# Optimization experiments

Measured on AMD Instinct MI355X. Metric: run time of the kernel, lower is better.

Reference implementation:

```python
import jax, jax.numpy as jnp
import numpy as np
import math

B, N, NBS, E, H = 64, 512, 8, 2048, 128
L, K = 3, 4
AF, BF = 82, 6
NA, NBTAB = 100, 10
ALPHA, LAMDA = 0.1, 0.5


def _gelu(x):
    return jax.nn.gelu(x, approximate=False)


def _mask_softmax(a, mask):
    # a: [..., n], mask broadcastable to a; matches torch mask_softmax (eps=1e-6)
    a_exp = jnp.exp(a - jnp.max(a, -1, keepdims=True)) * mask
    return a_exp / (jnp.sum(a_exp, -1, keepdims=True) + 1e-6)


def _gru(x, h, wih, whh, bih, bhh):
    # torch.nn.GRUCell semantics; wih/whh: [3H, H] in (r, z, n) order
    gi = x @ wih.T + bih
    gh = h @ whh.T + bhh
    ir, iz, inn = jnp.split(gi, 3, -1)
    hr, hz, hn = jnp.split(gh, 3, -1)
    r = jax.nn.sigmoid(ir + hr)
    z = jax.nn.sigmoid(iz + hz)
    n = jnp.tanh(inn + r * hn)
    return (1 - z) * n + z * h


def setup_inputs() -> dict:
    key = jax.random.key(0)
    ks = iter(jax.random.split(key, 64))
    def nrm(shape, s=0.05):
        return jax.random.normal(next(ks), shape, dtype=jnp.float32) * s
    def zb(shape):
        return jnp.zeros(shape, jnp.float32)
    inp = dict(
        batch_size=B,
        vertex_mask=jnp.ones((B, N), jnp.float32),
        vertex=jax.random.randint(next(ks), (B, N), 0, NA),
        edge=jax.random.randint(next(ks), (B, E), 0, NBTAB),
        atom_adj=jax.random.randint(next(ks), (B, N, NBS), 0, B * N),
        bond_adj=jax.random.randint(next(ks), (B, N, NBS), 0, B * E),
        nbs_mask=jnp.ones((B, N, NBS), jnp.float32),
        init_atom_features=nrm((NA, AF), 1.0),
        init_bond_features=nrm((NBTAB, BF), 1.0),
        emb_w=nrm((AF, H)), emb_b=zb((H,)),
        u1_w=nrm((L, H + BF, H)), u1_b=zb((L, H)),
        u2_w=nrm((L, 2 * H, H)), u2_b=zb((L, H)),
        fu_w=nrm((L, H, H)), fu_b=zb((L, H)),
        wvm_w=nrm((L, K, H, H)), wvm_b=zb((L, K, H)),
        wmain_w=nrm((L, K, H, H)), wmain_b=zb((L, K, H)),
        wbmm_w=nrm((L, K, H)), wbmm_b=zb((L, K)),
        khead_w=nrm((L, K * H, H)), khead_b=zb((L, H)),
        wmaster_w=nrm((L, H, H)), wmaster_b=zb((L, H)),
        wm2m_w=nrm((L, H, H)), wm2m_b=zb((L, H)),
        wzm1_w=nrm((L, H, H)), wzm1_b=zb((L, H)),
        wzm2_w=nrm((L, H, H)), wzm2_b=zb((L, H)),
        wzs1_w=nrm((L, H, H)), wzs1_b=zb((L, H)),
        wzs2_w=nrm((L, H, H)), wzs2_b=zb((L, H)),
        gru_main_wih=nrm((3 * H, H)), gru_main_whh=nrm((3 * H, H)),
        gru_main_bih=zb((3 * H,)), gru_main_bhh=zb((3 * H,)),
        gru_master_wih=nrm((3 * H, H)), gru_master_whh=nrm((3 * H, H)),
        gru_master_bih=zb((3 * H,)), gru_master_bhh=zb((3 * H,)),
    )
    return inp


def _compute(p, vertex, edge, atom_adj, bond_adj):
    vm = p['vertex_mask']               # [B, N]
    nm = p['nbs_mask']                  # [B, N, NBS]
    b, n_vertex = vm.shape
    nbs = atom_adj.shape[-1]
    # embed initial atom/bond features via table gather
    v_init = p['init_atom_features'][vertex.reshape(-1)].reshape(b, n_vertex, -1)
    e_init = p['init_bond_features'][edge.reshape(-1)].reshape(b, edge.shape[1], -1)
    v_init = v_init * vm[:, :, None]
    vf = _gelu(v_init @ p['emb_w'] + p['emb_b'])                       # [B, N, H]
    h0 = vf
    hdim = vf.shape[-1]
    master = jnp.sum(vf * vm[:, :, None], axis=1, keepdims=True)        # [B, 1, H]
    aa = atom_adj.reshape(-1)
    ba = bond_adj.reshape(-1)
    n_layers = p['u1_w'].shape[0]
    for i in range(n_layers):
        # --- multi-head main -> master attention (all heads vectorized) ---
        mv = jnp.tanh(jnp.einsum('bnh,khd->bknd', vf, p['wvm_w'][i]) + p['wvm_b'][i][None, :, None, :])
        score = jnp.einsum('bknd,kd->bkn', mv * master[:, None, :, :], p['wbmm_w'][i]) + p['wbmm_b'][i][None, :, None]
        att = _mask_softmax(score, vm[:, None, :])                      # [B, K, N]
        proj = jnp.einsum('bnh,khd->bknd', vf, p['wmain_w'][i]) + p['wmain_b'][i][None, :, None, :]
        kmm = jnp.einsum('bkn,bknd->bkd', att, proj)                    # [B, K, H]
        main_to_master = jnp.tanh(kmm.reshape(b, 1, -1) @ p['khead_w'][i] + p['khead_b'][i])  # [B, 1, H]
        # --- GraphConvolution (dropout p = 0.0) ---
        vn = vf.reshape(-1, hdim)[aa].reshape(b, n_vertex, nbs, hdim)
        en = e_init.reshape(-1, e_init.shape[-1])[ba].reshape(b, n_vertex, nbs, -1)
        lab = _gelu(jnp.concatenate([vn, en], -1) @ p['u1_w'][i] + p['u1_b'][i])
        nl = jnp.sum(lab * nm[..., None], axis=-2)                      # [B, N, H]
        hi = jnp.concatenate([nl, vf], -1) @ p['u2_w'][i] + p['u2_b'][i]
        theta = math.log(LAMDA / (i + 1) + 1)
        support = (1 - ALPHA) * hi + ALPHA * h0
        self_vertex = theta * (support @ p['fu_w'][i] + p['fu_b'][i]) + (1 - theta) * support
        # --- master updates + gated mixing + GRU cells ---
        m2m = _gelu(master @ p['wm2m_w'][i] + p['wm2m_b'][i])           # [B, 1, H]
        mself = _gelu(master @ p['wmaster_w'][i] + p['wmaster_b'][i])   # [B, 1, H]
        z_main = jax.nn.sigmoid(self_vertex @ p['wzm1_w'][i] + p['wzm1_b'][i] + m2m @ p['wzm2_w'][i] + p['wzm2_b'][i])
        hidden_main = (1 - z_main) * self_vertex + z_main * m2m          # broadcast [B,N,H]
        vf = _gru(hidden_main.reshape(-1, hdim), vf.reshape(-1, hdim),
                  p['gru_main_wih'], p['gru_main_whh'], p['gru_main_bih'], p['gru_main_bhh']).reshape(b, n_vertex, hdim)
        z_master = jax.nn.sigmoid(mself @ p['wzs1_w'][i] + p['wzs1_b'][i] + main_to_master @ p['wzs2_w'][i] + p['wzs2_b'][i])
        hidden_super = (1 - z_master) * mself + z_master * main_to_master
        master = _gru(hidden_super.reshape(b, hdim), master.reshape(b, hdim),
                      p['gru_master_wih'], p['gru_master_whh'], p['gru_master_bih'], p['gru_master_bhh']).reshape(b, 1, hdim)
    return vf, master


def reference(batch_size, vertex_mask, vertex, edge, atom_adj, bond_adj, nbs_mask,
              init_atom_features, init_bond_features, emb_w, emb_b,
              u1_w, u1_b, u2_w, u2_b, fu_w, fu_b,
              wvm_w, wvm_b, wmain_w, wmain_b, wbmm_w, wbmm_b, khead_w, khead_b,
              wmaster_w, wmaster_b, wm2m_w, wm2m_b,
              wzm1_w, wzm1_b, wzm2_w, wzm2_b, wzs1_w, wzs1_b, wzs2_w, wzs2_b,
              gru_main_wih, gru_main_whh, gru_main_bih, gru_main_bhh,
              gru_master_wih, gru_master_whh, gru_master_bih, gru_master_bhh):
    p = dict(vertex_mask=vertex_mask, nbs_mask=nbs_mask,
             init_atom_features=init_atom_features, init_bond_features=init_bond_features,
             emb_w=emb_w, emb_b=emb_b, u1_w=u1_w, u1_b=u1_b, u2_w=u2_w, u2_b=u2_b,
             fu_w=fu_w, fu_b=fu_b, wvm_w=wvm_w, wvm_b=wvm_b, wmain_w=wmain_w, wmain_b=wmain_b,
             wbmm_w=wbmm_w, wbmm_b=wbmm_b, khead_w=khead_w, khead_b=khead_b,
             wmaster_w=wmaster_w, wmaster_b=wmaster_b, wm2m_w=wm2m_w, wm2m_b=wm2m_b,
             wzm1_w=wzm1_w, wzm1_b=wzm1_b, wzm2_w=wzm2_w, wzm2_b=wzm2_b,
             wzs1_w=wzs1_w, wzs1_b=wzs1_b, wzs2_w=wzs2_w, wzs2_b=wzs2_b,
             gru_main_wih=gru_main_wih, gru_main_whh=gru_main_whh,
             gru_main_bih=gru_main_bih, gru_main_bhh=gru_main_bhh,
             gru_master_wih=gru_master_wih, gru_master_whh=gru_master_whh,
             gru_master_bih=gru_master_bih, gru_master_bhh=gru_master_bhh)
    return _compute(p, vertex, edge, atom_adj, bond_adj)
```

## Files before the change

kernel.cpp:

```cpp
#include <hip/hip_runtime.h>
#include <hip/hip_bf16.h>
#include <cmath>

#define BB 64
#define NN 512
#define NBS 8
#define EE 2048
#define HH 128
#define LL 3
#define KK 4
#define AF 82
#define BF 6
#define SLAB 4194304

typedef __attribute__((ext_vector_type(8))) short bf16x8;
typedef __attribute__((ext_vector_type(4))) float f32x4;

__device__ __forceinline__ float gelu1(float x){ return 0.5f*x*(1.f+erff(x*0.7071067811865475f)); }
__device__ __forceinline__ float sig1(float x){ return 1.f/(1.f+expf(-x)); }
__device__ __forceinline__ short f2bs(float x){ __hip_bfloat16 b=__float2bfloat16(x); return *reinterpret_cast<short*>(&b); }
__device__ __forceinline__ float bs2f(short s){ unsigned u = ((unsigned)(unsigned short)s) << 16; union{unsigned u; float f;} c; c.u=u; return c.f; }
__device__ __forceinline__ void split2(float v, short& hi, short& lo){ hi = f2bs(v); lo = f2bs(v - bs2f(hi)); }

#define MFMA3(ACC, AH, AL, BH, BL) \
// ... 41 lines not shown
                bf16x8 bl = *(const bf16x8*)(bp + 49152);
                MFMA3(acc[nt],   a0h[kc], a0l[kc], bh, bl);
                MFMA3(acc[8+nt], a1h[kc], a1l[kc], bh, bl);
            }
        }
        #pragma unroll
        for (int mt = 0; mt < 2; ++mt)
            #pragma unroll
            for (int nt = 0; nt < 8; ++nt) {
                int col = nt*16 + ml;
                #pragma unroll
                for (int r = 0; r < 4; ++r) {
                    int gm = m0 + mt*16 + quad*4 + r;
                    pvfb[(size_t)gm*128 + col] = f2bs(acc[mt*8+nt][r]);
                }
            }
    } else {
        const int v = bid - 256;
        const int k = v >> 8;
        const int tile = v & 255;
        const int b = tile >> 2;
        const int r0 = tile*128 + wv*32 + ml;
        const int r1 = r0 + 16;

        bf16x8 a0h[4], a0l[4], a1h[4], a1l[4];
        #pragma unroll
        for (int kc = 0; kc < 4; ++kc) {
            const int kq = kc*32 + quad*8;
            a0h[kc] = *(const bf16x8*)(vfh + (size_t)r0*128 + kq);
            a0l[kc] = *(const bf16x8*)(vfl + (size_t)r0*128 + kq);
            a1h[kc] = *(const bf16x8*)(vfh + (size_t)r1*128 + kq);
            a1l[kc] = *(const bf16x8*)(vfl + (size_t)r1*128 + kq);
        }
        f32x4 acc[16];
        #pragma unroll
        for (int i = 0; i < 16; ++i) acc[i] = (f32x4){0.f,0.f,0.f,0.f};
        const short* wcol = wtwvm + (size_t)k*16384 + (size_t)ml*128;
        #pragma unroll
        for (int kc = 0; kc < 4; ++kc) {
            const int kq = kc*32 + quad*8;
            #pragma unroll
            for (int nt = 0; nt < 8; ++nt) {
                const short* bp = wcol + (size_t)nt*16*128 + kq;
                bf16x8 bh = *(const bf16x8*)bp;
                bf16x8 bl = *(const bf16x8*)(bp + 196608);
                MFMA3(acc[nt],   a0h[kc], a0l[kc], bh, bl);
                MFMA3(acc[8+nt], a1h[kc], a1l[kc], bh, bl);
            }
        }
        float wv8[8], bj8[8];
        #pragma unroll
        for (int nt = 0; nt < 8; ++nt) {
            int col = nt*16 + ml;
            wv8[nt] = master[(size_t)b*128 + col] * wbw[(size_t)k*128 + col];
            bj8[nt] = wvmb[(size_t)k*128 + col];
        }
        float kb = wbb[k];
        #pragma unroll
        for (int mt = 0; mt < 2; ++mt) {
            #pragma unroll
            for (int r = 0; r < 4; ++r) {
                float s = 0.f;
                #pragma unroll
                for (int nt = 0; nt < 8; ++nt)
                    s += tanhf(acc[mt*8+nt][r] + bj8[nt]) * wv8[nt];
                s += __shfl_xor(s, 1); s += __shfl_xor(s, 2);
                s += __shfl_xor(s, 4); s += __shfl_xor(s, 8);
                if (ml == 0) {
                    int nloc = (tile & 3)*128 + wv*32 + mt*16 + quad*4 + r;
                    score[((size_t)(b*KK + k))*NN + nloc] = s + kb;
                }
            }
        }
    }
}

__global__ __launch_bounds__(256) void layer_k2(
    const short* __restrict__ pvfb, const float* __restrict__ pet,
    const int* __restrict__ aadj, const int* __restrict__ badj,
    const int* __restrict__ edge, const float* __restrict__ nbm,
    short* __restrict__ nlh, short* __restrict__ nll,
    const float* __restrict__ score, const float* __restrict__ vm,
    const float* __restrict__ vfc,
    float* __restrict__ satt, float* __restrict__ ctx)
{
    __shared__ float smem[768];
    const int bid = blockIdx.x;
    const int t = threadIdx.x;

    if (bid < 8192) {
        const int w = t >> 6, l = t & 63;
        const int i = bid*4 + w;
        const int sg = l >> 4, j = l & 15;
        float acc[8];
        #pragma unroll
        for (int c = 0; c < 8; ++c) acc[c] = 0.f;
        #pragma unroll
        for (int it = 0; it < 2; ++it) {
            int s = it*4 + sg;
            int flat = i*8 + s;
            int g = aadj[flat];
            int eid = edge[badj[flat]];
            float nv = nbm[flat];
            bf16x8 pv8 = *(const bf16x8*)(pvfb + (size_t)g*128 + j*8);
            const float* pp = pet + (size_t)eid*128 + j*8;
            float4 p0 = *(const float4*)pp, p1 = *(const float4*)(pp+4);
            float pe[8] = {p0.x,p0.y,p0.z,p0.w,p1.x,p1.y,p1.z,p1.w};
            #pragma unroll
            for (int c = 0; c < 8; ++c)
                acc[c] += gelu1(bs2f(pv8[c]) + pe[c]) * nv;
        }
        #pragma unroll
        for (int c = 0; c < 8; ++c) {
            acc[c] += __shfl_xor(acc[c], 16);
            acc[c] += __shfl_xor(acc[c], 32);
        }
        if (sg == 0) {
            short hs[8], ls[8];
            #pragma unroll
            for (int c = 0; c < 8; ++c) split2(acc[c], hs[c], ls[c]);
            size_t o = (size_t)i*128 + j*8;
            *(short4*)(nlh + o)     = make_short4(hs[0],hs[1],hs[2],hs[3]);
            *(short4*)(nlh + o + 4) = make_short4(hs[4],hs[5],hs[6],hs[7]);
            *(short4*)(nll + o)     = make_short4(ls[0],ls[1],ls[2],ls[3]);
            *(short4*)(nll + o + 4) = make_short4(ls[4],ls[5],ls[6],ls[7]);
        }
    } else {
        float* red = smem;
        float* att = smem + 256;
        const int bk = bid - 8192, b = bk >> 2;
        float v0 = score[(size_t)bk*NN + t], v1 = score[(size_t)bk*NN + 256 + t];
        red[t] = fmaxf(v0, v1); __syncthreads();
        for (int s = 128; s; s >>= 1) { if (t < s) red[t] = fmaxf(red[t], red[t+s]); __syncthreads(); }
        float mx = red[0]; __syncthreads();
        float e0 = expf(v0 - mx) * vm[b*NN + t];
        float e1 = expf(v1 - mx) * vm[b*NN + t + 256];
        red[t] = e0 + e1; __syncthreads();
        for (int s = 128; s; s >>= 1) { if (t < s) red[t] += red[t+s]; __syncthreads(); }
        float sum = red[0];
        float inv = 1.f / (sum + 1e-6f);
        att[t] = e0*inv; att[t+256] = e1*inv;
        if (t == 0) satt[bk] = sum*inv;
        __syncthreads();
        const int d = t & 127, h = t >> 7;
        float acc = 0.f;
        const float* V = vfc + (size_t)b*NN*HH;
        #pragma unroll 8
        for (int n = h*256; n < h*256 + 256; ++n) acc += att[n]*V[(size_t)n*HH + d];
        red[t] = acc; __syncthreads();
        if (t < 128) ctx[(size_t)bk*HH + t] = red[t] + red[t+128];
    }
}

__global__ __launch_bounds__(256, 2) void layer_k3(
    const short* __restrict__ nlh, const short* __restrict__ nll,
    const float* __restrict__ vfc, const short* __restrict__ vfch, const short* __restrict__ vfcl,
    float* __restrict__ vfn, short* __restrict__ vfnh, short* __restrict__ vfnl,
    const short* __restrict__ h0b,
    const short* __restrict__ wu2, const float* __restrict__ u2b,
    const short* __restrict__ wfu, const float* __restrict__ fub,
    const short* __restrict__ wbc, const float* __restrict__ zmb2v,
    const short* __restrict__ wih, const short* __restrict__ whh,
    const float* __restrict__ bih, const float* __restrict__ bhh,
    const float* __restrict__ t2, const float* __restrict__ m2m,
    float theta,
    const float* __restrict__ ctx, const float* __restrict__ satt,
    float* __restrict__ master,
    const float* __restrict__ wmain_w, const float* __restrict__ wmain_b,
    const float* __restrict__ khead_w, const float* __restrict__ khead_b,
    const float* __restrict__ wmaster_w, const float* __restrict__ wmaster_b,
    const float* __restrict__ wzs1_w,  const float* __restrict__ wzs1_b,
    const float* __restrict__ wzs2_w,  const float* __restrict__ wzs2_b,
    const float* __restrict__ WTih, const float* __restrict__ WThh,
    const float* __restrict__ bihm, const float* __restrict__ bhhm,
    const float* __restrict__ wm2m_n_w, const float* __restrict__ wm2m_n_b,
    const float* __restrict__ wzm2_n_w, const float* __restrict__ wzm2_n_b,
    float* __restrict__ m2m_out, float* __restrict__ t2_out)
{
    __shared__ __align__(16) char smem_raw[34816];
    const int bid = blockIdx.x;
    const int t = threadIdx.x;

    if (bid >= 64) {
        short* sh = (short*)smem_raw;
        short* sl = sh + 64*136;
        const int vb = bid - 64;
        const int lane = t & 63, wv = t >> 6;
        const int quad = lane >> 4, ml = lane & 15;
        const int base = vb * 64;
        const int bb = base >> 9;
        const int c0 = wv*32 + ml;
        const int c1 = c0 + 16;
        const int kq0 = quad*8;

        f32x4 acc[4][2];
        #pragma unroll
        for (int rt = 0; rt < 4; ++rt) {
            acc[rt][0] = (f32x4){0.f,0.f,0.f,0.f};
            acc[rt][1] = (f32x4){0.f,0.f,0.f,0.f};
        }

        #pragma unroll
        for (int kc = 0; kc < 4; ++kc) {
            const int kq = kc*32 + kq0;
            const short* bp0 = wu2 + (size_t)c0*256 + kq;
            const short* bp1 = wu2 + (size_t)c1*256 + kq;
            bf16x8 b0h = *(const bf16x8*)bp0, b0l = *(const bf16x8*)(bp0+98304);
            bf16x8 b1h = *(const bf16x8*)bp1, b1l = *(const bf16x8*)(bp1+98304);
            #pragma unroll
            for (int rt = 0; rt < 4; ++rt) {
                const size_t ar = (size_t)(base + rt*16 + ml);
                bf16x8 ah = *(const bf16x8*)(nlh + ar*128 + kq);
                bf16x8 al = *(const bf16x8*)(nll + ar*128 + kq);
                MFMA3(acc[rt][0], ah, al, b0h, b0l);
                MFMA3(acc[rt][1], ah, al, b1h, b1l);
            }
        }
        #pragma unroll
        for (int kc = 0; kc < 4; ++kc) {
            const int kq = kc*32 + kq0;
            const short* bp0 = wu2 + (size_t)c0*256 + 128 + kq;
            const short* bp1 = wu2 + (size_t)c1*256 + 128 + kq;
            bf16x8 b0h = *(const bf16x8*)bp0, b0l = *(const bf16x8*)(bp0+98304);
            bf16x8 b1h = *(const bf16x8*)bp1, b1l = *(const bf16x8*)(bp1+98304);
            #pragma unroll
            for (int rt = 0; rt < 4; ++rt) {
                const size_t ar = (size_t)(base + rt*16 + ml);
                bf16x8 ah = *(const bf16x8*)(vfch + ar*128 + kq);
                bf16x8 al = *(const bf16x8*)(vfcl + ar*128 + kq);
                MFMA3(acc[rt][0], ah, al, b0h, b0l);
                MFMA3(acc[rt][1], ah, al, b1h, b1l);
            }
        }
        f32x4 sup[4][2];
        {
            const float bj0 = u2b[c0], bj1 = u2b[c1];
            #pragma unroll
            for (int rt = 0; rt < 4; ++rt) {
                #pragma unroll
                for (int r = 0; r < 4; ++r) {
                    const size_t grow = (size_t)(base + rt*16 + quad*4 + r);
                    sup[rt][0][r] = 0.9f*(acc[rt][0][r]+bj0) + 0.1f*bs2f(h0b[grow*128 + c0]);
                    sup[rt][1][r] = 0.9f*(acc[rt][1][r]+bj1) + 0.1f*bs2f(h0b[grow*128 + c1]);
                    const int lrow = rt*16 + quad*4 + r;
                    short h_, l_;
                    split2(sup[rt][0][r], h_, l_); sh[lrow*136 + c0] = h_; sl[lrow*136 + c0] = l_;
                    split2(sup[rt][1][r], h_, l_); sh[lrow*136 + c1] = h_; sl[lrow*136 + c1] = l_;
                }
            }
        }
        __syncthreads();

        f32x4 accz[4][2];
        #pragma unroll
        for (int rt = 0; rt < 4; ++rt) {
            acc[rt][0] = (f32x4){0.f,0.f,0.f,0.f};
            acc[rt][1] = (f32x4){0.f,0.f,0.f,0.f};
            accz[rt][0] = (f32x4){0.f,0.f,0.f,0.f};
            accz[rt][1] = (f32x4){0.f,0.f,0.f,0.f};
        }
        #pragma unroll
        for (int kc = 0; kc < 4; ++kc) {
            const int kq = kc*32 + kq0;
            const short* bp0 = wfu + (size_t)c0*128 + kq;
            const short* bp1 = wfu + (size_t)c1*128 + kq;
            const short* zp0 = wbc + (size_t)c0*128 + kq;
            const short* zp1 = wbc + (size_t)c1*128 + kq;
            bf16x8 b0h = *(const bf16x8*)bp0, b0l = *(const bf16x8*)(bp0+49152);
            bf16x8 b1h = *(const bf16x8*)bp1, b1l = *(const bf16x8*)(bp1+49152);
            bf16x8 z0h = *(const bf16x8*)zp0, z0l = *(const bf16x8*)(zp0+49152);
            bf16x8 z1h = *(const bf16x8*)zp1, z1l = *(const bf16x8*)(zp1+49152);
            #pragma unroll
            for (int rt = 0; rt < 4; ++rt) {
                bf16x8 xh = *(const bf16x8*)&sh[(rt*16+ml)*136 + kq];
                bf16x8 xl = *(const bf16x8*)&sl[(rt*16+ml)*136 + kq];
                MFMA3(acc[rt][0], xh, xl, b0h, b0l);
                MFMA3(acc[rt][1], xh, xl, b1h, b1l);
                MFMA3(accz[rt][0], xh, xl, z0h, z0l);
                MFMA3(accz[rt][1], xh, xl, z1h, z1l);
            }
        }
        f32x4 hid[4][2];
        {
            const float bj0 = fub[c0], bj1 = fub[c1];
            const float zb0 = zmb2v[c0] + t2[(size_t)bb*128 + c0];
            const float zb1 = zmb2v[c1] + t2[(size_t)bb*128 + c1];
            const float m20 = m2m[(size_t)bb*128 + c0], m21 = m2m[(size_t)bb*128 + c1];
            #pragma unroll
            for (int rt = 0; rt < 4; ++rt) {
                #pragma unroll
                for (int r = 0; r < 4; ++r) {
                    float sv0 = theta*(acc[rt][0][r]+bj0) + (1.f-theta)*sup[rt][0][r];
                    float sv1 = theta*(acc[rt][1][r]+bj1) + (1.f-theta)*sup[rt][1][r];
                    float z0 = sig1(accz[rt][0][r] + zb0);
                    float z1 = sig1(accz[rt][1][r] + zb1);
                    hid[rt][0][r] = (1.f-z0)*sv0 + z0*m20;
                    hid[rt][1][r] = (1.f-z1)*sv1 + z1*m21;
                }
            }
        }
        __syncthreads();
        #pragma unroll
        for (int rt = 0; rt < 4; ++rt) {
            #pragma unroll
            for (int r = 0; r < 4; ++r) {
                const int lrow = rt*16 + quad*4 + r;
                short h_, l_;
                split2(hid[rt][0][r], h_, l_); sh[lrow*136 + c0] = h_; sl[lrow*136 + c0] = l_;
                split2(hid[rt][1][r], h_, l_); sh[lrow*136 + c1] = h_; sl[lrow*136 + c1] = l_;
            }
        }
        __syncthreads();

        f32x4 gr[4][2], gi[4][2], gh[4][2];
        #pragma unroll
        for (int rt = 0; rt < 4; ++rt) {
            gr[rt][0] = (f32x4){0.f,0.f,0.f,0.f};
            gr[rt][1] = (f32x4){0.f,0.f,0.f,0.f};
        }
        #pragma unroll
        for (int kc = 0; kc < 4; ++kc) {
            const int kq = kc*32 + kq0;
            const short* pw0 = wih + (size_t)c0*128 + kq;
            const short* pw1 = wih + (size_t)c1*128 + kq;
            const short* pu0 = whh + (size_t)c0*128 + kq;
            const short* pu1 = whh + (size_t)c1*128 + kq;
            bf16x8 w0h=*(const bf16x8*)pw0, w0l=*(const bf16x8*)(pw0+49152);
            bf16x8 w1h=*(const bf16x8*)pw1, w1l=*(const bf16x8*)(pw1+49152);
            bf16x8 u0h=*(const bf16x8*)pu0, u0l=*(const bf16x8*)(pu0+49152);
            bf16x8 u1h=*(const bf16x8*)pu1, u1l=*(const bf16x8*)(pu1+49152);
            #pragma unroll
            for (int rt = 0; rt < 4; ++rt) {
                const size_t ar = (size_t)(base + rt*16 + ml);
                bf16x8 xh = *(const bf16x8*)&sh[(rt*16+ml)*136 + kq];
                bf16x8 xl = *(const bf16x8*)&sl[(rt*16+ml)*136 + kq];
                bf16x8 hh = *(const bf16x8*)(vfch + ar*128 + kq);
                bf16x8 hl = *(const bf16x8*)(vfcl + ar*128 + kq);
                MFMA3(gr[rt][0], xh, xl, w0h, w0l);
                MFMA3(gr[rt][0], hh, hl, u0h, u0l);
                MFMA3(gr[rt][1], xh, xl, w1h, w1l);
                MFMA3(gr[rt][1], hh, hl, u1h, u1l);
            }
        }
        {
            const float br0 = bih[c0] + bhh[c0], br1 = bih[c1] + bhh[c1];
            #pragma unroll
            for (int rt = 0; rt < 4; ++rt) {
                #pragma unroll
                for (int r = 0; r < 4; ++r) {
                    gr[rt][0][r] = sig1(gr[rt][0][r] + br0);
                    gr[rt][1][r] = sig1(gr[rt][1][r] + br1);
                }
            }
        }
        #pragma unroll
        for (int rt = 0; rt < 4; ++rt) {
            gi[rt][0] = (f32x4){0.f,0.f,0.f,0.f};
            gi[rt][1] = (f32x4){0.f,0.f,0.f,0.f};
            gh[rt][0] = (f32x4){0.f,0.f,0.f,0.f};
            gh[rt][1] = (f32x4){0.f,0.f,0.f,0.f};
        }
        #pragma unroll
        for (int kc = 0; kc < 4; ++kc) {
            const int kq = kc*32 + kq0;
            const short* pw0 = wih + (size_t)(256 + c0)*128 + kq;
            const short* pw1 = wih + (size_t)(256 + c1)*128 + kq;
            const short* pu0 = whh + (size_t)(256 + c0)*128 + kq;
            const short* pu1 = whh + (size_t)(256 + c1)*128 + kq;
            bf16x8 w0h=*(const bf16x8*)pw0, w0l=*(const bf16x8*)(pw0+49152);
            bf16x8 w1h=*(const bf16x8*)pw1, w1l=*(const bf16x8*)(pw1+49152);
            bf16x8 u0h=*(const bf16x8*)pu0, u0l=*(const bf16x8*)(pu0+49152);
            bf16x8 u1h=*(const bf16x8*)pu1, u1l=*(const bf16x8*)(pu1+49152);
            #pragma unroll
            for (int rt = 0; rt < 4; ++rt) {
                const size_t ar = (size_t)(base + rt*16 + ml);
                bf16x8 xh = *(const bf16x8*)&sh[(rt*16+ml)*136 + kq];
                bf16x8 xl = *(const bf16x8*)&sl[(rt*16+ml)*136 + kq];
                bf16x8 hh = *(const bf16x8*)(vfch + ar*128 + kq);
                bf16x8 hl = *(const bf16x8*)(vfcl + ar*128 + kq);
                MFMA3(gi[rt][0], xh, xl, w0h, w0l);
                MFMA3(gh[rt][0], hh, hl, u0h, u0l);
                MFMA3(gi[rt][1], xh, xl, w1h, w1l);
                MFMA3(gh[rt][1], hh, hl, u1h, u1l);
            }
        }
        {
            const float bn0 = bih[256+c0], bn1 = bih[256+c1];
            const float un0 = bhh[256+c0], un1 = bhh[256+c1];
            #pragma unroll
            for (int rt = 0; rt < 4; ++rt) {
                #pragma unroll
                for (int r = 0; r < 4; ++r) {
                    gi[rt][0][r] = tanhf(gi[rt][0][r] + bn0 + gr[rt][0][r]*(gh[rt][0][r] + un0));
                    gi[rt][1][r] = tanhf(gi[rt][1][r] + bn1 + gr[rt][1][r]*(gh[rt][1][r] + un1));
                }
            }
        }
        #pragma unroll
        for (int rt = 0; rt < 4; ++rt) {
            gh[rt][0] = (f32x4){0.f,0.f,0.f,0.f};
            gh[rt][1] = (f32x4){0.f,0.f,0.f,0.f};
        }
        #pragma unroll
        for (int kc = 0; kc < 4; ++kc) {
            const int kq = kc*32 + kq0;
            const short* pw0 = wih + (size_t)(128 + c0)*128 + kq;
            const short* pw1 = wih + (size_t)(128 + c1)*128 + kq;
            const short* pu0 = whh + (size_t)(128 + c0)*128 + kq;
            const short* pu1 = whh + (size_t)(128 + c1)*128 + kq;
            bf16x8 w0h=*(const bf16x8*)pw0, w0l=*(const bf16x8*)(pw0+49152);
            bf16x8 w1h=*(const bf16x8*)pw1, w1l=*(const bf16x8*)(pw1+49152);
            bf16x8 u0h=*(const bf16x8*)pu0, u0l=*(const bf16x8*)(pu0+49152);
            bf16x8 u1h=*(const bf16x8*)pu1, u1l=*(const bf16x8*)(pu1+49152);
            #pragma unroll
            for (int rt = 0; rt < 4; ++rt) {
                const size_t ar = (size_t)(base + rt*16 + ml);
                bf16x8 xh = *(const bf16x8*)&sh[(rt*16+ml)*136 + kq];
                bf16x8 xl = *(const bf16x8*)&sl[(rt*16+ml)*136 + kq];
                bf16x8 hh = *(const bf16x8*)(vfch + ar*128 + kq);
                bf16x8 hl = *(const bf16x8*)(vfcl + ar*128 + kq);
                MFMA3(gh[rt][0], xh, xl, w0h, w0l);
                MFMA3(gh[rt][0], hh, hl, u0h, u0l);
                MFMA3(gh[rt][1], xh, xl, w1h, w1l);
                MFMA3(gh[rt][1], hh, hl, u1h, u1l);
            }
        }
        {
            const float bz0 = bih[128+c0] + bhh[128+c0];
            const float bz1 = bih[128+c1] + bhh[128+c1];
            #pragma unroll
            for (int rt = 0; rt < 4; ++rt) {
                #pragma unroll
                for (int r = 0; r < 4; ++r) {
                    const size_t grow = (size_t)(base + rt*16 + quad*4 + r);
                    const size_t off0 = grow*128 + c0, off1 = grow*128 + c1;
                    float z0 = sig1(gh[rt][0][r] + bz0);
                    float z1 = sig1(gh[rt][1][r] + bz1);
                    float o0 = (1.f-z0)*gi[rt][0][r] + z0*vfc[off0];
                    float o1 = (1.f-z1)*gi[rt][1][r] + z1*vfc[off1];
                    vfn[off0] = o0; vfn[off1] = o1;
                    short h_, l_;
                    split2(o0, h_, l_); vfnh[off0] = h_; vfnl[off0] = l_;
                    split2(o1, h_, l_); vfnh[off1] = h_; vfnl[off1] = l_;
                }
            }
        }
    } else {
        float* smemf = (float*)smem_raw;
        float* xs = smemf;
        float* ms = smemf + 512;
        float* msN = smemf + 640;
        float* v_mtm = smemf + 768;
        float* v_mself = smemf + 896;
        float* v_m2m = smemf + 1024;
        float* v_t2 = smemf + 1152;
        float* v_ts1 = smemf + 1280;
        float* v_ts2 = smemf + 1408;
        float* v_hsup = smemf + 1536;
        float* gi = smemf + 1664;
        float* gh2 = smemf + 2048;
        float* red = smemf + 2432;
        const int b = bid;

        if (t < 128) ms[t] = master[(size_t)b*128 + t];
        __syncthreads();

        const int c = t & 127, p = t >> 7;

        #pragma unroll
        for (int k = 0; k < 4; ++k) {
            const float* cx = ctx + ((size_t)b*KK + k)*128;
            const float* Wk = wmain_w + (size_t)k*16384;
            float s = 0.f;
            for (int d = p*64; d < p*64+64; ++d) s += cx[d]*Wk[(size_t)d*128 + c];
            red[t] = s; __syncthreads();
            if (t < 128) xs[k*128 + c] = red[c] + red[c+128] + satt[(size_t)b*KK + k]*wmain_b[k*128 + c];
            __syncthreads();
        }

        auto matvec = [&](const float* src, const float* __restrict__ W,
                          const float* __restrict__ bias, int K, float* out, int act) {
            int half = K >> 1;
            int k0 = p*half, k1 = k0 + half;
            float s = 0.f;
            for (int k = k0; k < k1; ++k) s += src[k]*W[(size_t)k*128 + c];
            red[t] = s; __syncthreads();
            if (t < 128) {
                float v = red[c] + red[c+128] + bias[c];
                if (act == 1) v = gelu1(v); else if (act == 2) v = tanhf(v);
                out[c] = v;
            }
            __syncthreads();
        };

        matvec(xs, khead_w, khead_b, 512, v_mtm, 2);
        matvec(ms, wmaster_w, wmaster_b, 128, v_mself, 1);
        matvec(v_mself, wzs1_w, wzs1_b, 128, v_ts1, 0);
        matvec(v_mtm, wzs2_w, wzs2_b, 128, v_ts2, 0);

        if (t < 128) {
            float z = sig1(v_ts1[t] + v_ts2[t]);
            v_hsup[t] = (1.f-z)*v_mself[t] + z*v_mtm[t];
        }
        __syncthreads();

        for (int j = t; j < 384; j += 256) {
            float a = 0.f, h2 = 0.f;
            for (int k = 0; k < 128; ++k) {
                a  += v_hsup[k]*WTih[(size_t)k*384 + j];
                h2 += ms[k]*WThh[(size_t)k*384 + j];
            }
            gi[j] = a + bihm[j];
            gh2[j] = h2 + bhhm[j];
        }
        __syncthreads();
        if (t < 128) {
            float r = sig1(gi[t] + gh2[t]);
            float z = sig1(gi[128+t] + gh2[128+t]);
            float n = tanhf(gi[256+t] + r*gh2[256+t]);
            float nm = (1.f-z)*n + z*ms[t];
            master[(size_t)b*128 + t] = nm;
            msN[t] = nm;
        }
        __syncthreads();

        matvec(msN, wm2m_n_w, wm2m_n_b, 128, v_m2m, 1);
        matvec(v_m2m, wzm2_n_w, wzm2_n_b, 128, v_t2, 0);
        if (t < 128) {
            m2m_out[(size_t)b*128 + t] = v_m2m[t];
            t2_out[(size_t)b*128 + t]  = v_t2[t];
        }
    }
}

__global__ __launch_bounds__(256) void embed_kernel(
    const float* __restrict__ atomf, const int* __restrict__ vertex,
    const float* __restrict__ vmask,
    const short* __restrict__ WT, const float* __restrict__ bias,
    float* __restrict__ vf, short* __restrict__ h0b,
    short* __restrict__ vfh, short* __restrict__ vfl)
{
    const int t = threadIdx.x;
    const int lane = t & 63, wv = t >> 6;
    const int quad = lane >> 4, ml = lane & 15;
    const int m0 = blockIdx.x*128 + wv*32;
    const int r0 = m0 + ml, r1 = m0 + 16 + ml;
    const int ga0 = vertex[r0], ga1 = vertex[r1];
    const float vm0 = vmask[r0], vm1 = vmask[r1];

    f32x4 acc[16];
    #pragma unroll
    for (int i = 0; i < 16; ++i) acc[i] = (f32x4){0.f,0.f,0.f,0.f};
    const short* wcol = WT + (size_t)ml*96;

    #pragma unroll
    for (int kc = 0; kc < 3; ++kc) {
        const int kq = kc*32 + quad*8;
        float av0[8], av1[8];
        const float* p0r = atomf + (size_t)ga0*AF + kq;
        const float* p1r = atomf + (size_t)ga1*AF + kq;
        #pragma unroll
        for (int j2 = 0; j2 < 4; ++j2) {
            int k = kq + 2*j2;
            if (k + 2 <= AF) {
                float2 v0 = *(const float2*)(p0r + 2*j2);
                float2 v1 = *(const float2*)(p1r + 2*j2);
                av0[2*j2]=v0.x*vm0; av0[2*j2+1]=v0.y*vm0;
                av1[2*j2]=v1.x*vm1; av1[2*j2+1]=v1.y*vm1;
            } else { av0[2*j2]=0.f; av0[2*j2+1]=0.f; av1[2*j2]=0.f; av1[2*j2+1]=0.f; }
        }
        bf16x8 a0h, a0l, a1h, a1l;
        #pragma unroll
        for (int j = 0; j < 8; ++j) {
            short h, l;
            split2(av0[j], h, l); a0h[j]=h; a0l[j]=l;
            split2(av1[j], h, l); a1h[j]=h; a1l[j]=l;
        }
        #pragma unroll
        for (int nt = 0; nt < 8; ++nt) {
            const short* bp = wcol + (size_t)nt*16*96 + kq;
            bf16x8 bh = *(const bf16x8*)bp;
            bf16x8 bl = *(const bf16x8*)(bp + 12288);
            MFMA3(acc[nt],   a0h, a0l, bh, bl);
            MFMA3(acc[8+nt], a1h, a1l, bh, bl);
        }
    }

    #pragma unroll
    for (int mt = 0; mt < 2; ++mt) {
        #pragma unroll
        for (int nt = 0; nt < 8; ++nt) {
            int col = nt*16 + ml;
            float bj = bias[col];
            #pragma unroll
            for (int r = 0; r < 4; ++r) {
                int gm = m0 + mt*16 + quad*4 + r;
                float v = gelu1(acc[mt*8+nt][r] + bj);
                size_t off = (size_t)gm*128 + col;
                vf[off] = v;
                short h_, l_; split2(v, h_, l_);
                vfh[off] = h_; vfl[off] = l_;
                h0b[off] = h_;
            }
        }
    }
}

__global__ __launch_bounds__(256) void master_init_a(
    const float* __restrict__ vf, const float* __restrict__ vm,
    float* __restrict__ master)
{
    __shared__ float red[256];
    const int bid = blockIdx.x;
    const int b = bid >> 3, sl = bid & 7;
    const int t = threadIdx.x;
    const int c = t & 127, half = t >> 7;
    float s = 0.f;
    for (int n = sl*64 + half; n < sl*64 + 64; n += 2)
        s += vf[((size_t)b*NN + n)*HH + c] * vm[b*NN + n];
    red[t] = s; __syncthreads();
    if (t < 128) atomicAdd(&master[(size_t)b*HH + c], red[c] + red[c+128]);
}

__global__ __launch_bounds__(256) void master_init_b(
    const float* __restrict__ master,
    const float* __restrict__ wm2m_w, const float* __restrict__ wm2m_b,
    const float* __restrict__ wzm2_w, const float* __restrict__ wzm2_b,
    float* __restrict__ m2m_out, float* __restrict__ t2_out)
{
    __shared__ float red[256], ms[128], v_m2m[128];
    const int b = blockIdx.x, t = threadIdx.x;
    if (t < 128) ms[t] = master[(size_t)b*HH + t];
    __syncthreads();
    const int c = t & 127, p = t >> 7;
    {
        float s2 = 0.f;
        for (int k = p*64; k < p*64+64; ++k) s2 += ms[k]*wm2m_w[(size_t)k*128 + c];
        red[t] = s2; __syncthreads();
        if (t < 128) { float v = gelu1(red[c] + red[c+128] + wm2m_b[c]); v_m2m[c] = v; m2m_out[(size_t)b*128 + c] = v; }
        __syncthreads();
    }
    {
        float s2 = 0.f;
        for (int k = p*64; k < p*64+64; ++k) s2 += v_m2m[k]*wzm2_w[(size_t)k*128 + c];
        red[t] = s2; __syncthreads();
        if (t < 128) t2_out[(size_t)b*128 + c] = red[c] + red[c+128] + wzm2_b[c];
    }
}

__device__ __forceinline__ void cvt_t2(const float* __restrict__ src, short* __restrict__ dst,
                                       int i, int K, int Kpad, int total, int zrows)
{
    int z = i / (128*Kpad); int rem = i - z*128*Kpad;
    int col = rem / Kpad; int k = rem - col*Kpad;
    float v = (k < K) ? src[(size_t)z*zrows*128 + (size_t)k*128 + col] : 0.f;
    short h, l; split2(v, h, l);
    dst[i] = h; dst[total + i] = l;
}

// ... 43 lines not shown
        const float* fu = fu_w + (size_t)li*16384 + (size_t)k*128;
        const float* wz = wzm1_w + (size_t)li*16384;
        float s = 0.f;
        for (int j = 0; j < 128; ++j) s += fu[j] * wz[(size_t)j*128 + c];
        s = theta*s + (1.f-theta)*wz[(size_t)k*128 + c];
        short h, lo; split2(s, h, lo);
        size_t d = (size_t)li*16384 + (size_t)c*128 + k;
        wt_wbc[d] = h; wt_wbc[49152 + d] = lo;
    }
    else if (i < 704640) {
        int o = i - 704256; int li = o >> 7; int c = o & 127;
        float theta = logf(0.5f/(float)(li+1) + 1.f);
        float s = 0.f;
        for (int j = 0; j < 128; ++j)
            s += fu_bv[li*128 + j] * wzm1_w[(size_t)li*16384 + (size_t)j*128 + c];
        zmb2[o] = wzm1_bv[li*128 + c] + theta*s;
    }
    else if (i < 712832) {
        master0[i - 704640] = 0.f;
    }
}

__global__ void copy_out_kernel(const float* __restrict__ vf, const float* __restrict__ master,
                                float* __restrict__ out)
{
    int i = blockIdx.x*256 + threadIdx.x;
    const int nvf4 = SLAB/4;
    if (i < nvf4) ((float4*)out)[i] = ((const float4*)vf)[i];
    else ((float4*)out)[i] = ((const float4*)master)[i - nvf4];
}

extern "C" void kernel_launch(void* const* d_in, const int* in_sizes, int n_in,
                              void* d_out, int out_size, void* d_ws, size_t ws_size,
                              hipStream_t stream)
{
    (void)in_sizes; (void)n_in; (void)out_size; (void)ws_size;
    const float* vmask = (const float*)d_in[1];
    const int*   vertex= (const int*)d_in[2];
    const int*   edge  = (const int*)d_in[3];
    const int*   aadj  = (const int*)d_in[4];
    const int*   badj  = (const int*)d_in[5];
    const float* nbm   = (const float*)d_in[6];
    const float* atomf = (const float*)d_in[7];
    const float* bondf = (const float*)d_in[8];
    const float* emb_w = (const float*)d_in[9];
    const float* emb_b = (const float*)d_in[10];
    const float* u1_w  = (const float*)d_in[11];
    const float* u1_b  = (const float*)d_in[12];
    const float* u2_w  = (const float*)d_in[13];
    const float* u2_b  = (const float*)d_in[14];
    const float* fu_w  = (const float*)d_in[15];
    const float* fu_b  = (const float*)d_in[16];
    const float* wvm_w = (const float*)d_in[17];
    const float* wvm_b = (const float*)d_in[18];
    const float* wmain_w=(const float*)d_in[19];
    const float* wmain_b=(const float*)d_in[20];
    const float* wbmm_w= (const float*)d_in[21];
    const float* wbmm_b= (const float*)d_in[22];
    const float* khead_w=(const float*)d_in[23];
    const float* khead_b=(const float*)d_in[24];
    const float* wmaster_w=(const float*)d_in[25];
    const float* wmaster_b=(const float*)d_in[26];
    const float* wm2m_w= (const float*)d_in[27];
    const float* wm2m_b= (const float*)d_in[28];
    const float* wzm1_w= (const float*)d_in[29];
    const float* wzm1_b= (const float*)d_in[30];
    const float* wzm2_w= (const float*)d_in[31];
    const float* wzm2_b= (const float*)d_in[32];
    const float* wzs1_w= (const float*)d_in[33];
    const float* wzs1_b= (const float*)d_in[34];
    const float* wzs2_w= (const float*)d_in[35];
    const float* wzs2_b= (const float*)d_in[36];
    const float* g_wih = (const float*)d_in[37];
    const float* g_whh = (const float*)d_in[38];
    const float* g_bih = (const float*)d_in[39];
    const float* g_bhh = (const float*)d_in[40];
    const float* gm_wih= (const float*)d_in[41];
    const float* gm_whh= (const float*)d_in[42];
    const float* gm_bih= (const float*)d_in[43];
    const float* gm_bhh= (const float*)d_in[44];

    float* ws     = (float*)d_ws;
    float* vfA    = ws;
    float* vfB    = vfA + SLAB;
    float* score  = vfB + SLAB;
    float* ctx    = score + BB*KK*NN;
    float* satt   = ctx + BB*KK*HH;
    float* master = satt + BB*KK;
    float* m2mA   = master + BB*HH;
    float* t2A    = m2mA + BB*HH;
    float* m2mB   = t2A + BB*HH;
    float* t2B    = m2mB + BB*HH;
    float* WTih_s = t2B + BB*HH;
    float* WThh_s = WTih_s + 128*384;
    float* pet    = WThh_s + 128*384;
    short* vfhA   = (short*)(pet + 3840);
    short* vflA   = vfhA + SLAB;
    short* vfhB   = vflA + SLAB;
    short* vflB   = vfhB + SLAB;
    short* nlh    = vflB + SLAB;
    short* nll    = nlh + SLAB;
    short* pvfb   = nll + SLAB;
    short* h0b    = pvfb + SLAB;
    short* wt_emb   = h0b + SLAB;
    short* wt_wvm   = wt_emb   + 2*12288;
    short* wt_pv    = wt_wvm   + 2*196608;
    short* wt_u2    = wt_pv    + 2*49152;
    short* wt_fu    = wt_u2    + 2*98304;
    short* wt_wzm1  = wt_fu    + 2*49152;
    short* wt_gih   = wt_wzm1  + 2*49152;
    short* wt_ghh   = wt_gih   + 2*49152;
    short* wt_wbc   = wt_ghh   + 2*49152;
    float* zmb2     = (float*)(wt_wbc + 2*49152);

    wprep_kernel<<<2785, 256, 0, stream>>>(
        emb_w, wvm_w, u1_w, u1_b, u2_w, fu_w, fu_b, wzm1_w, wzm1_b,
        g_wih, g_whh, gm_wih, gm_whh, bondf,
        wt_emb, wt_wvm, wt_pv, wt_u2, wt_fu, wt_wzm1, wt_gih, wt_ghh,
        wt_wbc, zmb2, WTih_s, WThh_s, pet, master);

    embed_kernel<<<256, 256, 0, stream>>>(atomf, vertex, vmask, wt_emb, emb_b,
                                          vfA, h0b, vfhA, vflA);

    master_init_a<<<512, 256, 0, stream>>>(vfA, vmask, master);
    master_init_b<<<BB, 256, 0, stream>>>(master, wm2m_w, wm2m_b, wzm2_w, wzm2_b,
                                          m2mA, t2A);

    for (int i = 0; i < LL; ++i) {
        float theta = logf(0.5f/(float)(i+1) + 1.f);
        const bool even = (i % 2 == 0);
        float* vfc  = even ? vfA  : vfB;
        short* vfch = even ? vfhA : vfhB;
        short* vfcl = even ? vflA : vflB;
        float* vfn  = even ? vfB  : vfA;
        short* vfnh = even ? vfhB : vfhA;
        short* vfnl = even ? vflB : vflA;
        float* m2mR = even ? m2mA : m2mB;
        float* t2R  = even ? t2A  : t2B;
        float* m2mW = even ? m2mB : m2mA;
        float* t2W  = even ? t2B  : t2A;
        int nx = (i+1 < LL) ? i+1 : i;

        layer_k1<<<1280, 256, 0, stream>>>(
            vfch, vfcl,
            wt_pv + (size_t)i*16384, pvfb,
            wt_wvm + (size_t)i*4*16384, wvm_b + (size_t)i*4*128,
            master, wbmm_w + (size_t)i*KK*HH, wbmm_b + (size_t)i*KK, score);

        layer_k2<<<8448, 256, 0, stream>>>(
            pvfb, pet + (size_t)i*1280,
            aadj, badj, edge, nbm, nlh, nll,
            score, vmask, vfc, satt, ctx);

        layer_k3<<<576, 256, 0, stream>>>(
            nlh, nll, vfc, vfch, vfcl, vfn, vfnh, vfnl, h0b,
            wt_u2 + (size_t)i*128*256, u2_b + i*HH,
            wt_fu + (size_t)i*16384, fu_b + i*HH,
            wt_wbc + (size_t)i*16384, zmb2 + i*HH,
            wt_gih, wt_ghh, g_bih, g_bhh,
            t2R, m2mR, theta,
            ctx, satt, master,
            wmain_w + (size_t)i*KK*HH*HH, wmain_b + (size_t)i*KK*HH,
            khead_w + (size_t)i*KK*HH*HH, khead_b + i*HH,
            wmaster_w + (size_t)i*HH*HH, wmaster_b + i*HH,
            wzs1_w + (size_t)i*HH*HH, wzs1_b + i*HH,
            wzs2_w + (size_t)i*HH*HH, wzs2_b + i*HH,
            WTih_s, WThh_s, gm_bih, gm_bhh,
            wm2m_w + (size_t)nx*HH*HH, wm2m_b + nx*HH,
            wzm2_w + (size_t)nx*HH*HH, wzm2_b + nx*HH,
            m2mW, t2W);
    }

    copy_out_kernel<<<(SLAB + BB*HH)/4/256, 256, 0, stream>>>(vfB, master, (float*)d_out);
}
```

Measured before the change: 783.0 us.

## Double layer_k3 block size so each wave computes one 16-column tile

layer_k3 now launches 512 threads per block instead of 256. In the MFMA path each of the eight waves computes one 16-column slice of the 64-row tile instead of two, which halves per-thread accumulator registers and spreads the weight loads over more waves. The master-node matvec path splits its K reduction four ways instead of two. This is meant to raise parallelism and latency hiding per block. In exchange, more waves share the same shared-memory activation loads, and the 34.8 KB shared buffer and red array must hold 512 entries.

```diff
diff --git a/kernel.cpp b/kernel.cpp
--- a/kernel.cpp
+++ b/kernel.cpp
@@ -217,7 +217,7 @@
     }
 }
 
-__global__ __launch_bounds__(256, 2) void layer_k3(
+__global__ __launch_bounds__(512) void layer_k3(
     const short* __restrict__ nlh, const short* __restrict__ nll,
     const float* __restrict__ vfc, const short* __restrict__ vfch, const short* __restrict__ vfcl,
     float* __restrict__ vfn, short* __restrict__ vfnh, short* __restrict__ vfnl,
@@ -254,113 +254,89 @@
         const int quad = lane >> 4, ml = lane & 15;
         const int base = vb * 64;
         const int bb = base >> 9;
-        const int c0 = wv*32 + ml;
-        const int c1 = c0 + 16;
+        const int c0 = wv*16 + ml;
         const int kq0 = quad*8;
 
-        f32x4 acc[4][2];
-        #pragma unroll
-        for (int rt = 0; rt < 4; ++rt) {
-            acc[rt][0] = (f32x4){0.f,0.f,0.f,0.f};
-            acc[rt][1] = (f32x4){0.f,0.f,0.f,0.f};
-        }
+        f32x4 acc[4];
+        #pragma unroll
+        for (int rt = 0; rt < 4; ++rt) acc[rt] = (f32x4){0.f,0.f,0.f,0.f};
 
         #pragma unroll
         for (int kc = 0; kc < 4; ++kc) {
             const int kq = kc*32 + kq0;
             const short* bp0 = wu2 + (size_t)c0*256 + kq;
-            const short* bp1 = wu2 + (size_t)c1*256 + kq;
             bf16x8 b0h = *(const bf16x8*)bp0, b0l = *(const bf16x8*)(bp0+98304);
-            bf16x8 b1h = *(const bf16x8*)bp1, b1l = *(const bf16x8*)(bp1+98304);
             #pragma unroll
             for (int rt = 0; rt < 4; ++rt) {
                 const size_t ar = (size_t)(base + rt*16 + ml);
                 bf16x8 ah = *(const bf16x8*)(nlh + ar*128 + kq);
                 bf16x8 al = *(const bf16x8*)(nll + ar*128 + kq);
-                MFMA3(acc[rt][0], ah, al, b0h, b0l);
-                MFMA3(acc[rt][1], ah, al, b1h, b1l);
+                MFMA3(acc[rt], ah, al, b0h, b0l);
             }
         }
         #pragma unroll
         for (int kc = 0; kc < 4; ++kc) {
             const int kq = kc*32 + kq0;
             const short* bp0 = wu2 + (size_t)c0*256 + 128 + kq;
-            const short* bp1 = wu2 + (size_t)c1*256 + 128 + kq;
             bf16x8 b0h = *(const bf16x8*)bp0, b0l = *(const bf16x8*)(bp0+98304);
-            bf16x8 b1h = *(const bf16x8*)bp1, b1l = *(const bf16x8*)(bp1+98304);
             #pragma unroll
             for (int rt = 0; rt < 4; ++rt) {
                 const size_t ar = (size_t)(base + rt*16 + ml);
                 bf16x8 ah = *(const bf16x8*)(vfch + ar*128 + kq);
                 bf16x8 al = *(const bf16x8*)(vfcl + ar*128 + kq);
-                MFMA3(acc[rt][0], ah, al, b0h, b0l);
-                MFMA3(acc[rt][1], ah, al, b1h, b1l);
-            }
-        }
-        f32x4 sup[4][2];
+                MFMA3(acc[rt], ah, al, b0h, b0l);
+            }
+        }
+        f32x4 sup[4];
         {
-            const float bj0 = u2b[c0], bj1 = u2b[c1];
+            const float bj0 = u2b[c0];
             #pragma unroll
             for (int rt = 0; rt < 4; ++rt) {
                 #pragma unroll
                 for (int r = 0; r < 4; ++r) {
                     const size_t grow = (size_t)(base + rt*16 + quad*4 + r);
-                    sup[rt][0][r] = 0.9f*(acc[rt][0][r]+bj0) + 0.1f*bs2f(h0b[grow*128 + c0]);
-                    sup[rt][1][r] = 0.9f*(acc[rt][1][r]+bj1) + 0.1f*bs2f(h0b[grow*128 + c1]);
+                    sup[rt][r] = 0.9f*(acc[rt][r]+bj0) + 0.1f*bs2f(h0b[grow*128 + c0]);
                     const int lrow = rt*16 + quad*4 + r;
                     short h_, l_;
-                    split2(sup[rt][0][r], h_, l_); sh[lrow*136 + c0] = h_; sl[lrow*136 + c0] = l_;
-                    split2(sup[rt][1][r], h_, l_); sh[lrow*136 + c1] = h_; sl[lrow*136 + c1] = l_;
+                    split2(sup[rt][r], h_, l_); sh[lrow*136 + c0] = h_; sl[lrow*136 + c0] = l_;
                 }
             }
         }
         __syncthreads();
 
-        f32x4 accz[4][2];
+        f32x4 accz[4];
         #pragma unroll
         for (int rt = 0; rt < 4; ++rt) {
-            acc[rt][0] = (f32x4){0.f,0.f,0.f,0.f};
-            acc[rt][1] = (f32x4){0.f,0.f,0.f,0.f};
-            accz[rt][0] = (f32x4){0.f,0.f,0.f,0.f};
-            accz[rt][1] = (f32x4){0.f,0.f,0.f,0.f};
+            acc[rt] = (f32x4){0.f,0.f,0.f,0.f};
+            accz[rt] = (f32x4){0.f,0.f,0.f,0.f};
         }
         #pragma unroll
         for (int kc = 0; kc < 4; ++kc) {
             const int kq = kc*32 + kq0;
             const short* bp0 = wfu + (size_t)c0*128 + kq;
-            const short* bp1 = wfu + (size_t)c1*128 + kq;
             const short* zp0 = wbc + (size_t)c0*128 + kq;
-            const short* zp1 = wbc + (size_t)c1*128 + kq;
             bf16x8 b0h = *(const bf16x8*)bp0, b0l = *(const bf16x8*)(bp0+49152);
-            bf16x8 b1h = *(const bf16x8*)bp1, b1l = *(const bf16x8*)(bp1+49152);
             bf16x8 z0h = *(const bf16x8*)zp0, z0l = *(const bf16x8*)(zp0+49152);
-            bf16x8 z1h = *(const bf16x8*)zp1, z1l = *(const bf16x8*)(zp1+49152);
             #pragma unroll
             for (int rt = 0; rt < 4; ++rt) {
                 bf16x8 xh = *(const bf16x8*)&sh[(rt*16+ml)*136 + kq];
                 bf16x8 xl = *(const bf16x8*)&sl[(rt*16+ml)*136 + kq];
-                MFMA3(acc[rt][0], xh, xl, b0h, b0l);
-                MFMA3(acc[rt][1], xh, xl, b1h, b1l);
-                MFMA3(accz[rt][0], xh, xl, z0h, z0l);
-                MFMA3(accz[rt][1], xh, xl, z1h, z1l);
-            }
-        }
-        f32x4 hid[4][2];
+                MFMA3(acc[rt], xh, xl, b0h, b0l);
+                MFMA3(accz[rt], xh, xl, z0h, z0l);
+            }
+        }
+        f32x4 hid[4];
         {
-            const float bj0 = fub[c0], bj1 = fub[c1];
+            const float bj0 = fub[c0];
             const float zb0 = zmb2v[c0] + t2[(size_t)bb*128 + c0];
-            const float zb1 = zmb2v[c1] + t2[(size_t)bb*128 + c1];
-            const float m20 = m2m[(size_t)bb*128 + c0], m21 = m2m[(size_t)bb*128 + c1];
+            const float m20 = m2m[(size_t)bb*128 + c0];
             #pragma unroll
             for (int rt = 0; rt < 4; ++rt) {
                 #pragma unroll
                 for (int r = 0; r < 4; ++r) {
-                    float sv0 = theta*(acc[rt][0][r]+bj0) + (1.f-theta)*sup[rt][0][r];
-                    float sv1 = theta*(acc[rt][1][r]+bj1) + (1.f-theta)*sup[rt][1][r];
-                    float z0 = sig1(accz[rt][0][r] + zb0);
-                    float z1 = sig1(accz[rt][1][r] + zb1);
-                    hid[rt][0][r] = (1.f-z0)*sv0 + z0*m20;
-                    hid[rt][1][r] = (1.f-z1)*sv1 + z1*m21;
+                    float sv0 = theta*(acc[rt][r]+bj0) + (1.f-theta)*sup[rt][r];
+                    float z0 = sig1(accz[rt][r] + zb0);
+                    hid[rt][r] = (1.f-z0)*sv0 + z0*m20;
                 }
             }
         }
@@ -371,29 +347,21 @@
             for (int r = 0; r < 4; ++r) {
                 const int lrow = rt*16 + quad*4 + r;
                 short h_, l_;
-                split2(hid[rt][0][r], h_, l_); sh[lrow*136 + c0] = h_; sl[lrow*136 + c0] = l_;
-                split2(hid[rt][1][r], h_, l_); sh[lrow*136 + c1] = h_; sl[lrow*136 + c1] = l_;
+                split2(hid[rt][r], h_, l_); sh[lrow*136 + c0] = h_; sl[lrow*136 + c0] = l_;
             }
         }
         __syncthreads();
 
-        f32x4 gr[4][2], gi[4][2], gh[4][2];
-        #pragma unroll
-        for (int rt = 0; rt < 4; ++rt) {
-            gr[rt][0] = (f32x4){0.f,0.f,0.f,0.f};
-            gr[rt][1] = (f32x4){0.f,0.f,0.f,0.f};
-        }
+        f32x4 gr[4], gi[4], gh[4];
+        #pragma unroll
+        for (int rt = 0; rt < 4; ++rt) gr[rt] = (f32x4){0.f,0.f,0.f,0.f};
         #pragma unroll
         for (int kc = 0; kc < 4; ++kc) {
             const int kq = kc*32 + kq0;
             const short* pw0 = wih + (size_t)c0*128 + kq;
-            const short* pw1 = wih + (size_t)c1*128 + kq;
             const short* pu0 = whh + (size_t)c0*128 + kq;
-            const short* pu1 = whh + (size_t)c1*128 + kq;
             bf16x8 w0h=*(const bf16x8*)pw0, w0l=*(const bf16x8*)(pw0+49152);
-            bf16x8 w1h=*(const bf16x8*)pw1, w1l=*(const bf16x8*)(pw1+49152);
             bf16x8 u0h=*(const bf16x8*)pu0, u0l=*(const bf16x8*)(pu0+49152);
-            bf16x8 u1h=*(const bf16x8*)pu1, u1l=*(const bf16x8*)(pu1+49152);
             #pragma unroll
             for (int rt = 0; rt < 4; ++rt) {
                 const size_t ar = (size_t)(base + rt*16 + ml);
@@ -401,41 +369,30 @@
                 bf16x8 xl = *(const bf16x8*)&sl[(rt*16+ml)*136 + kq];
                 bf16x8 hh = *(const bf16x8*)(vfch + ar*128 + kq);
                 bf16x8 hl = *(const bf16x8*)(vfcl + ar*128 + kq);
-                MFMA3(gr[rt][0], xh, xl, w0h, w0l);
-                MFMA3(gr[rt][0], hh, hl, u0h, u0l);
-                MFMA3(gr[rt][1], xh, xl, w1h, w1l);
-                MFMA3(gr[rt][1], hh, hl, u1h, u1l);
+                MFMA3(gr[rt], xh, xl, w0h, w0l);
+                MFMA3(gr[rt], hh, hl, u0h, u0l);
             }
         }
         {
-            const float br0 = bih[c0] + bhh[c0], br1 = bih[c1] + bhh[c1];
-            #pragma unroll
-            for (int rt = 0; rt < 4; ++rt) {
+            const float br0 = bih[c0] + bhh[c0];
+            #pragma unroll
+            for (int rt = 0; rt < 4; ++rt)
                 #pragma unroll
-                for (int r = 0; r < 4; ++r) {
-                    gr[rt][0][r] = sig1(gr[rt][0][r] + br0);
-                    gr[rt][1][r] = sig1(gr[rt][1][r] + br1);
-                }
-            }
+                for (int r = 0; r < 4; ++r)
+                    gr[rt][r] = sig1(gr[rt][r] + br0);
         }
         #pragma unroll
         for (int rt = 0; rt < 4; ++rt) {
-            gi[rt][0] = (f32x4){0.f,0.f,0.f,0.f};
-            gi[rt][1] = (f32x4){0.f,0.f,0.f,0.f};
-            gh[rt][0] = (f32x4){0.f,0.f,0.f,0.f};
-            gh[rt][1] = (f32x4){0.f,0.f,0.f,0.f};
+            gi[rt] = (f32x4){0.f,0.f,0.f,0.f};
+            gh[rt] = (f32x4){0.f,0.f,0.f,0.f};
         }
         #pragma unroll
         for (int kc = 0; kc < 4; ++kc) {
             const int kq = kc*32 + kq0;
             const short* pw0 = wih + (size_t)(256 + c0)*128 + kq;
-            const short* pw1 = wih + (size_t)(256 + c1)*128 + kq;
             const short* pu0 = whh + (size_t)(256 + c0)*128 + kq;
-            const short* pu1 = whh + (size_t)(256 + c1)*128 + kq;
             bf16x8 w0h=*(const bf16x8*)pw0, w0l=*(const bf16x8*)(pw0+49152);
-            bf16x8 w1h=*(const bf16x8*)pw1, w1l=*(const bf16x8*)(pw1+49152);
             bf16x8 u0h=*(const bf16x8*)pu0, u0l=*(const bf16x8*)(pu0+49152);
-            bf16x8 u1h=*(const bf16x8*)pu1, u1l=*(const bf16x8*)(pu1+49152);
             #pragma unroll
             for (int rt = 0; rt < 4; ++rt) {
                 const size_t ar = (size_t)(base + rt*16 + ml);
@@ -443,40 +400,28 @@
                 bf16x8 xl = *(const bf16x8*)&sl[(rt*16+ml)*136 + kq];
                 bf16x8 hh = *(const bf16x8*)(vfch + ar*128 + kq);
                 bf16x8 hl = *(const bf16x8*)(vfcl + ar*128 + kq);
-                MFMA3(gi[rt][0], xh, xl, w0h, w0l);
-                MFMA3(gh[rt][0], hh, hl, u0h, u0l);
-                MFMA3(gi[rt][1], xh, xl, w1h, w1l);
-                MFMA3(gh[rt][1], hh, hl, u1h, u1l);
+                MFMA3(gi[rt], xh, xl, w0h, w0l);
+                MFMA3(gh[rt], hh, hl, u0h, u0l);
             }
         }
         {
-            const float bn0 = bih[256+c0], bn1 = bih[256+c1];
-            const float un0 = bhh[256+c0], un1 = bhh[256+c1];
-            #pragma unroll
-            for (int rt = 0; rt < 4; ++rt) {
+            const float bn0 = bih[256+c0];
+            const float un0 = bhh[256+c0];
+            #pragma unroll
+            for (int rt = 0; rt < 4; ++rt)
                 #pragma unroll
-                for (int r = 0; r < 4; ++r) {
-                    gi[rt][0][r] = tanhf(gi[rt][0][r] + bn0 + gr[rt][0][r]*(gh[rt][0][r] + un0));
-                    gi[rt][1][r] = tanhf(gi[rt][1][r] + bn1 + gr[rt][1][r]*(gh[rt][1][r] + un1));
-                }
-            }
-        }
-        #pragma unroll
-        for (int rt = 0; rt < 4; ++rt) {
-            gh[rt][0] = (f32x4){0.f,0.f,0.f,0.f};
-            gh[rt][1] = (f32x4){0.f,0.f,0.f,0.f};
-        }
+                for (int r = 0; r < 4; ++r)
+                    gi[rt][r] = tanhf(gi[rt][r] + bn0 + gr[rt][r]*(gh[rt][r] + un0));
+        }
+        #pragma unroll
+        for (int rt = 0; rt < 4; ++rt) gh[rt] = (f32x4){0.f,0.f,0.f,0.f};
         #pragma unroll
         for (int kc = 0; kc < 4; ++kc) {
             const int kq = kc*32 + kq0;
             const short* pw0 = wih + (size_t)(128 + c0)*128 + kq;
-            const short* pw1 = wih + (size_t)(128 + c1)*128 + kq;
             const short* pu0 = whh + (size_t)(128 + c0)*128 + kq;
-            const short* pu1 = whh + (size_t)(128 + c1)*128 + kq;
             bf16x8 w0h=*(const bf16x8*)pw0, w0l=*(const bf16x8*)(pw0+49152);
-            bf16x8 w1h=*(const bf16x8*)pw1, w1l=*(const bf16x8*)(pw1+49152);
             bf16x8 u0h=*(const bf16x8*)pu0, u0l=*(const bf16x8*)(pu0+49152);
-            bf16x8 u1h=*(const bf16x8*)pu1, u1l=*(const bf16x8*)(pu1+49152);
             #pragma unroll
             for (int rt = 0; rt < 4; ++rt) {
                 const size_t ar = (size_t)(base + rt*16 + ml);
@@ -484,29 +429,23 @@
                 bf16x8 xl = *(const bf16x8*)&sl[(rt*16+ml)*136 + kq];
                 bf16x8 hh = *(const bf16x8*)(vfch + ar*128 + kq);
                 bf16x8 hl = *(const bf16x8*)(vfcl + ar*128 + kq);
-                MFMA3(gh[rt][0], xh, xl, w0h, w0l);
-                MFMA3(gh[rt][0], hh, hl, u0h, u0l);
-                MFMA3(gh[rt][1], xh, xl, w1h, w1l);
-                MFMA3(gh[rt][1], hh, hl, u1h, u1l);
+                MFMA3(gh[rt], xh, xl, w0h, w0l);
+                MFMA3(gh[rt], hh, hl, u0h, u0l);
             }
         }
         {
             const float bz0 = bih[128+c0] + bhh[128+c0];
-            const float bz1 = bih[128+c1] + bhh[128+c1];
             #pragma unroll
             for (int rt = 0; rt < 4; ++rt) {
                 #pragma unroll
                 for (int r = 0; r < 4; ++r) {
                     const size_t grow = (size_t)(base + rt*16 + quad*4 + r);
-                    const size_t off0 = grow*128 + c0, off1 = grow*128 + c1;
-                    float z0 = sig1(gh[rt][0][r] + bz0);
-                    float z1 = sig1(gh[rt][1][r] + bz1);
-                    float o0 = (1.f-z0)*gi[rt][0][r] + z0*vfc[off0];
-                    float o1 = (1.f-z1)*gi[rt][1][r] + z1*vfc[off1];
-                    vfn[off0] = o0; vfn[off1] = o1;
+                    const size_t off0 = grow*128 + c0;
+                    float z0 = sig1(gh[rt][r] + bz0);
+                    float o0 = (1.f-z0)*gi[rt][r] + z0*vfc[off0];
+                    vfn[off0] = o0;
                     short h_, l_;
                     split2(o0, h_, l_); vfnh[off0] = h_; vfnl[off0] = l_;
-                    split2(o1, h_, l_); vfnh[off1] = h_; vfnl[off1] = l_;
                 }
             }
         }
@@ -537,21 +476,22 @@
             const float* cx = ctx + ((size_t)b*KK + k)*128;
             const float* Wk = wmain_w + (size_t)k*16384;
             float s = 0.f;
-            for (int d = p*64; d < p*64+64; ++d) s += cx[d]*Wk[(size_t)d*128 + c];
+            for (int d = p*32; d < p*32+32; ++d) s += cx[d]*Wk[(size_t)d*128 + c];
             red[t] = s; __syncthreads();
-            if (t < 128) xs[k*128 + c] = red[c] + red[c+128] + satt[(size_t)b*KK + k]*wmain_b[k*128 + c];
+            if (t < 128) xs[k*128 + c] = red[c] + red[c+128] + red[c+256] + red[c+384]
+                                         + satt[(size_t)b*KK + k]*wmain_b[k*128 + c];
             __syncthreads();
         }
 
         auto matvec = [&](const float* src, const float* __restrict__ W,
                           const float* __restrict__ bias, int K, float* out, int act) {
-            int half = K >> 1;
-            int k0 = p*half, k1 = k0 + half;
+            int quarter = K >> 2;
+            int k0 = p*quarter, k1 = k0 + quarter;
             float s = 0.f;
             for (int k = k0; k < k1; ++k) s += src[k]*W[(size_t)k*128 + c];
             red[t] = s; __syncthreads();
             if (t < 128) {
-                float v = red[c] + red[c+128] + bias[c];
+                float v = red[c] + red[c+128] + red[c+256] + red[c+384] + bias[c];
                 if (act == 1) v = gelu1(v); else if (act == 2) v = tanhf(v);
                 out[c] = v;
             }
@@ -569,7 +509,7 @@
         }
         __syncthreads();
 
-        for (int j = t; j < 384; j += 256) {
+        for (int j = t; j < 384; j += 512) {
             float a = 0.f, h2 = 0.f;
             for (int k = 0; k < 128; ++k) {
                 a  += v_hsup[k]*WTih[(size_t)k*384 + j];
@@ -919,7 +859,7 @@
             aadj, badj, edge, nbm, nlh, nll,
             score, vmask, vfc, satt, ctx);
 
-        layer_k3<<<576, 256, 0, stream>>>(
+        layer_k3<<<576, 512, 0, stream>>>(
             nlh, nll, vfc, vfch, vfcl, vfn, vfnh, vfnl, h0b,
             wt_u2 + (size_t)i*128*256, u2_b + i*HH,
             wt_fu + (size_t)i*16384, fu_b + i*HH,
```

Result: slower. 943.9 us (+20.6%).
